# Kernel optimization log

Hardware: AMD Instinct MI355X
Metric: run time of the kernel (lower is better)

Reference implementation:

```python
import jax, jax.numpy as jnp
import numpy as np

NEG_SLOPE = 0.2

def leaky(x):
    return jnp.where(x >= 0, x, NEG_SLOPE * x)

def setup_inputs() -> dict:
    key = jax.random.key(0)
    ks = jax.random.split(key, 9)
    B, D, H = 2048, 128, 512
    s = lambda fan: 1.0 / np.sqrt(fan)
    return {
        "x":   jax.random.normal(ks[0], (B, D), jnp.float32),
        "We1": jax.random.normal(ks[1], (H, D), jnp.float32) * s(D),
        "be1": jax.random.normal(ks[2], (H,), jnp.float32) * s(D),
        "We2": jax.random.normal(ks[3], (D, H), jnp.float32) * s(H),
        "be2": jax.random.normal(ks[4], (D,), jnp.float32) * s(H),
        "W1s": jax.random.normal(ks[5], (D, H), jnp.float32),      # dec_j.linear1 weight (H,1) stacked -> (D,H)
        "b1s": jax.random.normal(ks[6], (D, H), jnp.float32) * 0.1,
        "W2s": jax.random.normal(ks[7], (D, D, H), jnp.float32) * s(H),  # dec_j.linear2 weight (D,H) stacked
        "b2s": jax.random.normal(ks[8], (D, D), jnp.float32) * s(H),
    }

def reference(x, We1, be1, We2, be2, W1s, b1s, W2s, b2s):
    # Encoder: D -> H -> D, tanh
    enc_h = leaky(x @ We1.T + be1)                     # (B,H)
    encoded = jnp.tanh(enc_h @ We2.T + be2)            # (B,D)
    # Per-feature decoders, vectorized over j: dec_j(encoded[:, j])
    z = encoded.T                                      # (D,B) latent scalar per decoder j
    hid = leaky(z[:, :, None] * W1s[:, None, :] + b1s[:, None, :])   # (D,B,H)
    terms = jnp.einsum('jbh,jdh->jbd', hid, W2s) + b2s[:, None, :]   # (D,B,D)
    # outputs[i] = sum_{j<=i} terms[j] -> inclusive prefix sum over j
    outputs = jnp.tanh(jnp.cumsum(terms, axis=0))      # (D,B,D)
    return outputs
```

## Files before the change

### kernel.cpp

```cpp
#include <hip/hip_runtime.h>

#define B_SZ 2048
#define D_SZ 128
#define H_SZ 512
#define JC 8
#define NCH 16
#define CPG 3
#define NGRP 5

typedef _Float16 half8 __attribute__((ext_vector_type(8)));
typedef float floatx4 __attribute__((ext_vector_type(4)));
typedef unsigned int uint4v __attribute__((ext_vector_type(4)));

static __device__ __forceinline__ float tanh_fast(float x) {
  float e = __expf(2.0f * x);
  return 1.0f - 2.0f * __builtin_amdgcn_rcpf(e + 1.0f);
}

static __device__ __forceinline__ void split_pair(float a, float b,
                                                  unsigned int& hi,
                                                  unsigned int& lo) {
  auto h = __builtin_amdgcn_cvt_pkrtz(a, b);
  float ra = a - (float)h[0];
  float rb = b - (float)h[1];
  auto l = __builtin_amdgcn_cvt_pkrtz(ra, rb);
  hi = __builtin_bit_cast(unsigned int, h);
  lo = __builtin_bit_cast(unsigned int, l);
}

__global__ __launch_bounds__(256) void prep_kernel(
    const float* __restrict__ W2s, _Float16* __restrict__ W2h,
    _Float16* __restrict__ W2l, const float* __restrict__ x,
    const float* __restrict__ We1, const float* __restrict__ be1,
    const float* __restrict__ We2, const float* __restrict__ be2,
    float* __restrict__ z) {
  const int t = threadIdx.x;
  if (blockIdx.x >= 256) {
    const int idx = (blockIdx.x - 256) * 256 + t;
    const int dl = idx & 63, kg = (idx >> 6) & 63, dtj = idx >> 12;
    const int d = (dtj & 1) * 64 + dl, j = dtj >> 1;
    const float* src = W2s + ((size_t)j * D_SZ + d) * H_SZ + kg * 8;
    float4 a = *(const float4*)src;
    float4 b = *(const float4*)(src + 4);
    unsigned int h0, l0, h1, l1, h2, l2, h3, l3;
    split_pair(a.x, a.y, h0, l0); split_pair(a.z, a.w, h1, l1);
    split_pair(b.x, b.y, h2, l2); split_pair(b.z, b.w, h3, l3);
    ((uint4*)W2h)[idx] = make_uint4(h0, h1, h2, h3);
    ((uint4*)W2l)[idx] = make_uint4(l0, l1, l2, l3);
    return;
  }
  __shared__ float xs[8][132];
  __shared__ float hs[8][516];
  const int b0 = blockIdx.x * 8;
  {
    int r = t >> 5, c4 = t & 31;
    float4 v = ((const float4*)(x + (size_t)(b0 + r) * D_SZ))[c4];
    xs[r][c4 * 4 + 0] = v.x; xs[r][c4 * 4 + 1] = v.y;
    xs[r][c4 * 4 + 2] = v.z; xs[r][c4 * 4 + 3] = v.w;
  }
  __syncthreads();
  for (int hb = 0; hb < 2; ++hb) {
    const int h = t + hb * 256;
    float acc[8];
    float bias = be1[h];
#pragma unroll
    for (int r = 0; r < 8; ++r) acc[r] = bias;
    const float4* wp = (const float4*)(We1 + (size_t)h * D_SZ);
    for (int k4 = 0; k4 < 32; ++k4) {
      float4 wv = wp[k4];
#pragma unroll
      for (int r = 0; r < 8; ++r) {
        acc[r] = fmaf(wv.x, xs[r][k4 * 4 + 0], acc[r]);
        acc[r] = fmaf(wv.y, xs[r][k4 * 4 + 1], acc[r]);
        acc[r] = fmaf(wv.z, xs[r][k4 * 4 + 2], acc[r]);
        acc[r] = fmaf(wv.w, xs[r][k4 * 4 + 3], acc[r]);
      }
    }
#pragma unroll
    for (int r = 0; r < 8; ++r) {
      float u = acc[r];
      hs[r][h] = fmaxf(u, 0.2f * u);
    }
  }
  __syncthreads();
  {
    const int d = t & 127, rg = t >> 7;
    float acc[4];
    float bias = be2[d];
#pragma unroll
    for (int r = 0; r < 4; ++r) acc[r] = bias;
    const float4* wp = (const float4*)(We2 + (size_t)d * H_SZ);
    for (int k4 = 0; k4 < 128; ++k4) {
      float4 wv = wp[k4];
#pragma unroll
      for (int r = 0; r < 4; ++r) {
        int row = rg * 4 + r;
        acc[r] = fmaf(wv.x, hs[row][k4 * 4 + 0], acc[r]);
        acc[r] = fmaf(wv.y, hs[row][k4 * 4 + 1], acc[r]);
        acc[r] = fmaf(wv.z, hs[row][k4 * 4 + 2], acc[r]);
        acc[r] = fmaf(wv.w, hs[row][k4 * 4 + 3], acc[r]);
      }
    }
#pragma unroll
    for (int r = 0; r < 4; ++r) {
      z[(size_t)d * B_SZ + b0 + rg * 4 + r] = tanh_fast(acc[r]);
    }
  }
}

__global__ __launch_bounds__(256, 2) void dec_kernel(
    const float* __restrict__ W1s, const float* __restrict__ b1s,
    const _Float16* __restrict__ W2h, const _Float16* __restrict__ W2l,
    const float* __restrict__ b2s, const float* __restrict__ z,
    float* __restrict__ out, float* __restrict__ T) {
  __shared__ float w1L[JC][512];
  __shared__ float b1L[JC][512];
  __shared__ float zL[JC][64];
  __shared__ float b2L[JC][128];
  __shared__ uint4v aHs[2][4][64];
  __shared__ uint4v aLs[2][4][64];

  const int t = threadIdx.x, bx = blockIdx.x;
  const int jc = bx & 15, bt = bx >> 4;
  const int b0 = bt * 64, j0 = jc * JC;

#pragma unroll
  for (int i = 0; i < 4; ++i) {
    int g = t + 256 * i;
    int jr = g >> 7, col = (g & 127) * 4;
    *(float4*)&w1L[jr][col] = *(const float4*)(W1s + (size_t)(j0 + jr) * H_SZ + col);
    *(float4*)&b1L[jr][col] = *(const float4*)(b1s + (size_t)(j0 + jr) * H_SZ + col);
  }
  if (t < 128) {
    int jr = t >> 4, col = (t & 15) * 4;
    *(float4*)&zL[jr][col] = *(const float4*)(z + (size_t)(j0 + jr) * B_SZ + b0 + col);
  }
  {
    int jr = t >> 5, col = (t & 31) * 4;
    *(float4*)&b2L[jr][col] = *(const float4*)(b2s + (size_t)(j0 + jr) * D_SZ + col);
  }
  __syncthreads();

  const int lane = t & 63;
  const int quad = lane >> 4, l16 = lane & 15;
  const int w = t >> 6;
  const int h = w & 1;
  const int pw = w ^ 1;

  floatx4 acc[2][4][3];
#pragma unroll
  for (int a = 0; a < 2; ++a)
#pragma unroll
    for (int b = 0; b < 4; ++b)
#pragma unroll
      for (int p = 0; p < 3; ++p) acc[a][b][p] = (floatx4){0.f, 0.f, 0.f, 0.f};
  float bc[4] = {0.f, 0.f, 0.f, 0.f};

  for (int jj = 0; jj < JC; ++jj) {
    const int j = j0 + jj;
    const unsigned int bb0 =
        (unsigned)(j * 2 + h) * 32768u + (unsigned)(quad * 512 + l16 * 8);
    const float zv = zL[jj][w * 16 + l16];

#pragma unroll 2
    for (int ks = 0; ks < 16; ++ks) {
      const int par = ks & 1;
      const unsigned int off = bb0 + (unsigned)(ks * 2048);
      half8 fh0 = *(const half8*)(W2h + off);
      half8 fh1 = *(const half8*)(W2h + off + 128);
      half8 fh2 = *(const half8*)(W2h + off + 256);
      half8 fh3 = *(const half8*)(W2h + off + 384);
      half8 fl0 = *(const half8*)(W2l + off);
      half8 fl1 = *(const half8*)(W2l + off + 128);
      half8 fl2 = *(const half8*)(W2l + off + 256);
      half8 fl3 = *(const half8*)(W2l + off + 384);

      const int ko = ks * 32 + quad * 8;
      float4 wa = *(const float4*)&w1L[jj][ko];
      float4 wc = *(const float4*)&w1L[jj][ko + 4];
      float4 ba = *(const float4*)&b1L[jj][ko];
      float4 bb = *(const float4*)&b1L[jj][ko + 4];

      float h0 = fmaf(zv, wa.x, ba.x), h1 = fmaf(zv, wa.y, ba.y);
      float h2 = fmaf(zv, wa.z, ba.z), h3 = fmaf(zv, wa.w, ba.w);
      float h4 = fmaf(zv, wc.x, bb.x), h5 = fmaf(zv, wc.y, bb.y);
      float h6 = fmaf(zv, wc.z, bb.z), h7 = fmaf(zv, wc.w, bb.w);
      h0 = fmaxf(h0, 0.2f * h0); h1 = fmaxf(h1, 0.2f * h1);
      h2 = fmaxf(h2, 0.2f * h2); h3 = fmaxf(h3, 0.2f * h3);
      h4 = fmaxf(h4, 0.2f * h4); h5 = fmaxf(h5, 0.2f * h5);
      h6 = fmaxf(h6, 0.2f * h6); h7 = fmaxf(h7, 0.2f * h7);
      unsigned int a0, a1, a2, a3, x0, x1, x2, x3;
      split_pair(h0, h1, a0, x0); split_pair(h2, h3, a1, x1);
      split_pair(h4, h5, a2, x2); split_pair(h6, h7, a3, x3);
      half8 fah = __builtin_bit_cast(half8, (uint4v){a0, a1, a2, a3});
      half8 fal = __builtin_bit_cast(half8, (uint4v){x0, x1, x2, x3});

      aHs[par][w][lane] = (uint4v){a0, a1, a2, a3};
      aLs[par][w][lane] = (uint4v){x0, x1, x2, x3};
      __syncthreads();
      half8 pah = __builtin_bit_cast(half8, aHs[par][pw][lane]);
      half8 pal = __builtin_bit_cast(half8, aLs[par][pw][lane]);

      acc[0][0][0] = __builtin_amdgcn_mfma_f32_16x16x32_f16(fah, fh0, acc[0][0][0], 0, 0, 0);
      acc[0][0][1] = __builtin_amdgcn_mfma_f32_16x16x32_f16(fah, fl0, acc[0][0][1], 0, 0, 0);
      acc[0][0][2] = __builtin_amdgcn_mfma_f32_16x16x32_f16(fal, fh0, acc[0][0][2], 0, 0, 0);
      acc[0][1][0] = __builtin_amdgcn_mfma_f32_16x16x32_f16(fah, fh1, acc[0][1][0], 0, 0, 0);
      acc[0][1][1] = __builtin_amdgcn_mfma_f32_16x16x32_f16(fah, fl1, acc[0][1][1], 0, 0, 0);
      acc[0][1][2] = __builtin_amdgcn_mfma_f32_16x16x32_f16(fal, fh1, acc[0][1][2], 0, 0, 0);
      acc[0][2][0] = __builtin_amdgcn_mfma_f32_16x16x32_f16(fah, fh2, acc[0][2][0], 0, 0, 0);
      acc[0][2][1] = __builtin_amdgcn_mfma_f32_16x16x32_f16(fah, fl2, acc[0][2][1], 0, 0, 0);
      acc[0][2][2] = __builtin_amdgcn_mfma_f32_16x16x32_f16(fal, fh2, acc[0][2][2], 0, 0, 0);
      acc[0][3][0] = __builtin_amdgcn_mfma_f32_16x16x32_f16(fah, fh3, acc[0][3][0], 0, 0, 0);
      acc[0][3][1] = __builtin_amdgcn_mfma_f32_16x16x32_f16(fah, fl3, acc[0][3][1], 0, 0, 0);
      acc[0][3][2] = __builtin_amdgcn_mfma_f32_16x16x32_f16(fal, fh3, acc[0][3][2], 0, 0, 0);
      acc[1][0][0] = __builtin_amdgcn_mfma_f32_16x16x32_f16(pah, fh0, acc[1][0][0], 0, 0, 0);
      acc[1][0][1] = __builtin_amdgcn_mfma_f32_16x16x32_f16(pah, fl0, acc[1][0][1], 0, 0, 0);
      acc[1][0][2] = __builtin_amdgcn_mfma_f32_16x16x32_f16(pal, fh0, acc[1][0][2], 0, 0, 0);
      acc[1][1][0] = __builtin_amdgcn_mfma_f32_16x16x32_f16(pah, fh1, acc[1][1][0], 0, 0, 0);
      acc[1][1][1] = __builtin_amdgcn_mfma_f32_16x16x32_f16(pah, fl1, acc[1][1][1], 0, 0, 0);
      acc[1][1][2] = __builtin_amdgcn_mfma_f32_16x16x32_f16(pal, fh1, acc[1][1][2], 0, 0, 0);
      acc[1][2][0] = __builtin_amdgcn_mfma_f32_16x16x32_f16(pah, fh2, acc[1][2][0], 0, 0, 0);
      acc[1][2][1] = __builtin_amdgcn_mfma_f32_16x16x32_f16(pah, fl2, acc[1][2][1], 0, 0, 0);
      acc[1][2][2] = __builtin_amdgcn_mfma_f32_16x16x32_f16(pal, fh2, acc[1][2][2], 0, 0, 0);
      acc[1][3][0] = __builtin_amdgcn_mfma_f32_16x16x32_f16(pah, fh3, acc[1][3][0], 0, 0, 0);
      acc[1][3][1] = __builtin_amdgcn_mfma_f32_16x16x32_f16(pah, fl3, acc[1][3][1], 0, 0, 0);
      acc[1][3][2] = __builtin_amdgcn_mfma_f32_16x16x32_f16(pal, fh3, acc[1][3][2], 0, 0, 0);
    }

#pragma unroll
    for (int df = 0; df < 4; ++df) bc[df] += b2L[jj][h * 64 + df * 16 + l16];

    const int dcol = h * 64 + l16;
    float* obase = out + (size_t)j * (B_SZ * D_SZ) + dcol;
#pragma unroll
    for (int bf = 0; bf < 2; ++bf) {
      const int rb = bf ? pw : w;
      const int brow = b0 + rb * 16 + quad * 4;
      float* orow = obase + (size_t)brow * D_SZ;
#pragma unroll
      for (int r = 0; r < 4; ++r) {
#pragma unroll
        for (int df = 0; df < 4; ++df) {
          float s = (acc[bf][df][0][r] + acc[bf][df][1][r]) +
                    (acc[bf][df][2][r] + bc[df]);
          if (jc == 0) s = tanh_fast(s);
          orow[(size_t)r * D_SZ + df * 16] = s;
        }
      }
    }
  }

  if (jc < NCH - 1) {
    const int dcol = h * 64 + l16;
    float* tbase = T + (size_t)jc * (B_SZ * D_SZ) + dcol;
#pragma unroll
    for (int bf = 0; bf < 2; ++bf) {
      const int rb = bf ? pw : w;
      const int brow = b0 + rb * 16 + quad * 4;
      float* trow = tbase + (size_t)brow * D_SZ;
#pragma unroll
      for (int r = 0; r < 4; ++r) {
#pragma unroll
        for (int df = 0; df < 4; ++df) {
          trow[(size_t)r * D_SZ + df * 16] =
              (acc[bf][df][0][r] + acc[bf][df][1][r]) +
              (acc[bf][df][2][r] + bc[df]);
        }
      }
    }
  }
}

__global__ __launch_bounds__(256) void fixup_kernel(
    const float* __restrict__ T, float* __restrict__ out) {
  const int idx = blockIdx.x * 256 + threadIdx.x;
  const int d4 = idx & 31;
  const int b = (idx >> 5) & (B_SZ - 1);
  const int q = idx >> 16;
  const size_t stride = B_SZ * (D_SZ / 4);
  const size_t tix = (size_t)b * (D_SZ / 4) + d4;
  const float4* T4 = (const float4*)T;
  float4* O4 = (float4*)out;

  const int c0 = 1 + q * CPG;
  float4 carry = make_float4(0.f, 0.f, 0.f, 0.f);
  for (int c = 0; c < c0; ++c) {
    float4 tv = T4[(size_t)c * stride + tix];
    carry.x += tv.x; carry.y += tv.y; carry.z += tv.z; carry.w += tv.w;
  }
#pragma unroll
  for (int cc = 0; cc < CPG; ++cc) {
    const int c = c0 + cc;
    if (cc > 0) {
      float4 tv = T4[(size_t)(c - 1) * stride + tix];
      carry.x += tv.x; carry.y += tv.y; carry.z += tv.z; carry.w += tv.w;
    }
#pragma unroll
    for (int jj = 0; jj < JC; ++jj) {
      const int j = c * JC + jj;
      const size_t oix = ((size_t)j * B_SZ + b) * (D_SZ / 4) + d4;
      float4 s = O4[oix];
      s.x = tanh_fast(s.x + carry.x);
      s.y = tanh_fast(s.y + carry.y);
      s.z = tanh_fast(s.z + carry.z);
      s.w = tanh_fast(s.w + carry.w);
      O4[oix] = s;
    }
  }
}

extern "C" void kernel_launch(void* const* d_in, const int* in_sizes, int n_in,
                              void* d_out, int out_size, void* d_ws,
                              size_t ws_size, hipStream_t stream) {
  (void)in_sizes; (void)n_in; (void)out_size; (void)ws_size;
  const float* x   = (const float*)d_in[0];
  const float* We1 = (const float*)d_in[1];
  const float* be1 = (const float*)d_in[2];
  const float* We2 = (const float*)d_in[3];
  const float* be2 = (const float*)d_in[4];
  const float* W1s = (const float*)d_in[5];
  const float* b1s = (const float*)d_in[6];
  const float* W2s = (const float*)d_in[7];
  const float* b2s = (const float*)d_in[8];
  float* out = (float*)d_out;

  float* zws = (float*)d_ws;
  _Float16* W2h = (_Float16*)((char*)d_ws + (1u << 20));
  _Float16* W2l = (_Float16*)((char*)d_ws + (1u << 20) + (1u << 24));
  float* T = (float*)((char*)d_ws + (1u << 20) + (2u << 24));

  prep_kernel<<<4352, 256, 0, stream>>>(W2s, W2h, W2l, x, We1, be1, We2, be2, zws);
  dec_kernel<<<512, 256, 0, stream>>>(W1s, b1s, W2h, W2l, b2s, zws, out, T);
  fixup_kernel<<<NGRP * 256, 256, 0, stream>>>(T, out);
}
```

Baseline: 340.8 us.

## Software-pipeline W2 fragment loads across flattened j/k loop and merge accumulators

Flattens the per-decoder and k-step loops into one 128-step loop and prefetches the next step's W2 hi/lo fragments and activation split one iteration ahead, so global loads and LDS exchange overlap the MFMAs of the current step. The two low-order correction accumulators are merged into one, cutting accumulator registers from 24 to 16 floatx4 sets, though the prefetch buffers add register pressure. The single barrier per step now covers the double-buffered LDS activation exchange for the next step.

```diff
diff --git a/kernel.cpp b/kernel.cpp
--- a/kernel.cpp
+++ b/kernel.cpp
@@ -146,41 +146,82 @@
   const int w = t >> 6;
   const int h = w & 1;
   const int pw = w ^ 1;
-
-  floatx4 acc[2][4][3];
+  const int rowL = w * 16 + l16;
+  const unsigned voff = (unsigned)(quad * 512 + l16 * 8);
+
+  floatx4 acc[2][4][2];
 #pragma unroll
   for (int a = 0; a < 2; ++a)
 #pragma unroll
     for (int b = 0; b < 4; ++b)
 #pragma unroll
-      for (int p = 0; p < 3; ++p) acc[a][b][p] = (floatx4){0.f, 0.f, 0.f, 0.f};
+      for (int p = 0; p < 2; ++p) acc[a][b][p] = (floatx4){0.f, 0.f, 0.f, 0.f};
   float bc[4] = {0.f, 0.f, 0.f, 0.f};
 
-  for (int jj = 0; jj < JC; ++jj) {
+  half8 curh, curl, cb[8];
+  {
+    const float zv = zL[0][rowL];
+    const int ko = quad * 8;
+    float4 wa = *(const float4*)&w1L[0][ko];
+    float4 wc = *(const float4*)&w1L[0][ko + 4];
+    float4 ba = *(const float4*)&b1L[0][ko];
+    float4 bb = *(const float4*)&b1L[0][ko + 4];
+    float h0 = fmaf(zv, wa.x, ba.x), h1 = fmaf(zv, wa.y, ba.y);
+    float h2 = fmaf(zv, wa.z, ba.z), h3 = fmaf(zv, wa.w, ba.w);
+    float h4 = fmaf(zv, wc.x, bb.x), h5 = fmaf(zv, wc.y, bb.y);
+    float h6 = fmaf(zv, wc.z, bb.z), h7 = fmaf(zv, wc.w, bb.w);
+    h0 = fmaxf(h0, 0.2f * h0); h1 = fmaxf(h1, 0.2f * h1);
+    h2 = fmaxf(h2, 0.2f * h2); h3 = fmaxf(h3, 0.2f * h3);
+    h4 = fmaxf(h4, 0.2f * h4); h5 = fmaxf(h5, 0.2f * h5);
+    h6 = fmaxf(h6, 0.2f * h6); h7 = fmaxf(h7, 0.2f * h7);
+    unsigned int a0, a1, a2, a3, x0, x1, x2, x3;
+    split_pair(h0, h1, a0, x0); split_pair(h2, h3, a1, x1);
+    split_pair(h4, h5, a2, x2); split_pair(h6, h7, a3, x3);
+    aHs[0][w][lane] = (uint4v){a0, a1, a2, a3};
+    aLs[0][w][lane] = (uint4v){x0, x1, x2, x3};
+    curh = __builtin_bit_cast(half8, (uint4v){a0, a1, a2, a3});
+    curl = __builtin_bit_cast(half8, (uint4v){x0, x1, x2, x3});
+    const unsigned off = (unsigned)(j0 * 2 + h) * 32768u + voff;
+    cb[0] = *(const half8*)(W2h + off);
+    cb[1] = *(const half8*)(W2h + off + 128);
+    cb[2] = *(const half8*)(W2h + off + 256);
+    cb[3] = *(const half8*)(W2h + off + 384);
+    cb[4] = *(const half8*)(W2l + off);
+    cb[5] = *(const half8*)(W2l + off + 128);
+    cb[6] = *(const half8*)(W2l + off + 256);
+    cb[7] = *(const half8*)(W2l + off + 384);
+  }
+  __syncthreads();
+
+#pragma unroll 2
+  for (int s = 0; s < 128; ++s) {
+    const int par = s & 1;
+    const int jj = s >> 4;
     const int j = j0 + jj;
-    const unsigned int bb0 =
-        (unsigned)(j * 2 + h) * 32768u + (unsigned)(quad * 512 + l16 * 8);
-    const float zv = zL[jj][w * 16 + l16];
-
-#pragma unroll 2
-    for (int ks = 0; ks < 16; ++ks) {
-      const int par = ks & 1;
-      const unsigned int off = bb0 + (unsigned)(ks * 2048);
-      half8 fh0 = *(const half8*)(W2h + off);
-      half8 fh1 = *(const half8*)(W2h + off + 128);
-      half8 fh2 = *(const half8*)(W2h + off + 256);
-      half8 fh3 = *(const half8*)(W2h + off + 384);
-      half8 fl0 = *(const half8*)(W2l + off);
-      half8 fl1 = *(const half8*)(W2l + off + 128);
-      half8 fl2 = *(const half8*)(W2l + off + 256);
-      half8 fl3 = *(const half8*)(W2l + off + 384);
-
-      const int ko = ks * 32 + quad * 8;
-      float4 wa = *(const float4*)&w1L[jj][ko];
-      float4 wc = *(const float4*)&w1L[jj][ko + 4];
-      float4 ba = *(const float4*)&b1L[jj][ko];
-      float4 bb = *(const float4*)&b1L[jj][ko + 4];
-
+
+    uint4v pH = aHs[par][pw][lane];
+    uint4v pL = aLs[par][pw][lane];
+
+    half8 nb[8], nh, nl;
+    if (s < 127) {
+      const int sn = s + 1;
+      const int jn = sn >> 4, kn = sn & 15;
+      const unsigned off = (unsigned)((j0 + jn) * 2 + h) * 32768u +
+                           (unsigned)(kn * 2048) + voff;
+      nb[0] = *(const half8*)(W2h + off);
+      nb[1] = *(const half8*)(W2h + off + 128);
+      nb[2] = *(const half8*)(W2h + off + 256);
+      nb[3] = *(const half8*)(W2h + off + 384);
+      nb[4] = *(const half8*)(W2l + off);
+      nb[5] = *(const half8*)(W2l + off + 128);
+      nb[6] = *(const half8*)(W2l + off + 256);
+      nb[7] = *(const half8*)(W2l + off + 384);
+      const float zv = zL[jn][rowL];
+      const int ko = kn * 32 + quad * 8;
+      float4 wa = *(const float4*)&w1L[jn][ko];
+      float4 wc = *(const float4*)&w1L[jn][ko + 4];
+      float4 ba = *(const float4*)&b1L[jn][ko];
+      float4 bb = *(const float4*)&b1L[jn][ko + 4];
       float h0 = fmaf(zv, wa.x, ba.x), h1 = fmaf(zv, wa.y, ba.y);
       float h2 = fmaf(zv, wa.z, ba.z), h3 = fmaf(zv, wa.w, ba.w);
       float h4 = fmaf(zv, wc.x, bb.x), h5 = fmaf(zv, wc.y, bb.y);
@@ -192,59 +233,49 @@
       unsigned int a0, a1, a2, a3, x0, x1, x2, x3;
       split_pair(h0, h1, a0, x0); split_pair(h2, h3, a1, x1);
       split_pair(h4, h5, a2, x2); split_pair(h6, h7, a3, x3);
-      half8 fah = __builtin_bit_cast(half8, (uint4v){a0, a1, a2, a3});
-      half8 fal = __builtin_bit_cast(half8, (uint4v){x0, x1, x2, x3});
-
-      aHs[par][w][lane] = (uint4v){a0, a1, a2, a3};
-      aLs[par][w][lane] = (uint4v){x0, x1, x2, x3};
-      __syncthreads();
-      half8 pah = __builtin_bit_cast(half8, aHs[par][pw][lane]);
-      half8 pal = __builtin_bit_cast(half8, aLs[par][pw][lane]);
-
-      acc[0][0][0] = __builtin_amdgcn_mfma_f32_16x16x32_f16(fah, fh0, acc[0][0][0], 0, 0, 0);
-      acc[0][0][1] = __builtin_amdgcn_mfma_f32_16x16x32_f16(fah, fl0, acc[0][0][1], 0, 0, 0);
-      acc[0][0][2] = __builtin_amdgcn_mfma_f32_16x16x32_f16(fal, fh0, acc[0][0][2], 0, 0, 0);
-      acc[0][1][0] = __builtin_amdgcn_mfma_f32_16x16x32_f16(fah, fh1, acc[0][1][0], 0, 0, 0);
-      acc[0][1][1] = __builtin_amdgcn_mfma_f32_16x16x32_f16(fah, fl1, acc[0][1][1], 0, 0, 0);
-      acc[0][1][2] = __builtin_amdgcn_mfma_f32_16x16x32_f16(fal, fh1, acc[0][1][2], 0, 0, 0);
-      acc[0][2][0] = __builtin_amdgcn_mfma_f32_16x16x32_f16(fah, fh2, acc[0][2][0], 0, 0, 0);
-      acc[0][2][1] = __builtin_amdgcn_mfma_f32_16x16x32_f16(fah, fl2, acc[0][2][1], 0, 0, 0);
-      acc[0][2][2] = __builtin_amdgcn_mfma_f32_16x16x32_f16(fal, fh2, acc[0][2][2], 0, 0, 0);
-      acc[0][3][0] = __builtin_amdgcn_mfma_f32_16x16x32_f16(fah, fh3, acc[0][3][0], 0, 0, 0);
-      acc[0][3][1] = __builtin_amdgcn_mfma_f32_16x16x32_f16(fah, fl3, acc[0][3][1], 0, 0, 0);
-      acc[0][3][2] = __builtin_amdgcn_mfma_f32_16x16x32_f16(fal, fh3, acc[0][3][2], 0, 0, 0);
-      acc[1][0][0] = __builtin_amdgcn_mfma_f32_16x16x32_f16(pah, fh0, acc[1][0][0], 0, 0, 0);
-      acc[1][0][1] = __builtin_amdgcn_mfma_f32_16x16x32_f16(pah, fl0, acc[1][0][1], 0, 0, 0);
-      acc[1][0][2] = __builtin_amdgcn_mfma_f32_16x16x32_f16(pal, fh0, acc[1][0][2], 0, 0, 0);
-      acc[1][1][0] = __builtin_amdgcn_mfma_f32_16x16x32_f16(pah, fh1, acc[1][1][0], 0, 0, 0);
-      acc[1][1][1] = __builtin_amdgcn_mfma_f32_16x16x32_f16(pah, fl1, acc[1][1][1], 0, 0, 0);
-      acc[1][1][2] = __builtin_amdgcn_mfma_f32_16x16x32_f16(pal, fh1, acc[1][1][2], 0, 0, 0);
-      acc[1][2][0] = __builtin_amdgcn_mfma_f32_16x16x32_f16(pah, fh2, acc[1][2][0], 0, 0, 0);
-      acc[1][2][1] = __builtin_amdgcn_mfma_f32_16x16x32_f16(pah, fl2, acc[1][2][1], 0, 0, 0);
-      acc[1][2][2] = __builtin_amdgcn_mfma_f32_16x16x32_f16(pal, fh2, acc[1][2][2], 0, 0, 0);
-      acc[1][3][0] = __builtin_amdgcn_mfma_f32_16x16x32_f16(pah, fh3, acc[1][3][0], 0, 0, 0);
-      acc[1][3][1] = __builtin_amdgcn_mfma_f32_16x16x32_f16(pah, fl3, acc[1][3][1], 0, 0, 0);
-      acc[1][3][2] = __builtin_amdgcn_mfma_f32_16x16x32_f16(pal, fh3, acc[1][3][2], 0, 0, 0);
-    }
-
-#pragma unroll
-    for (int df = 0; df < 4; ++df) bc[df] += b2L[jj][h * 64 + df * 16 + l16];
-
-    const int dcol = h * 64 + l16;
-    float* obase = out + (size_t)j * (B_SZ * D_SZ) + dcol;
-#pragma unroll
-    for (int bf = 0; bf < 2; ++bf) {
-      const int rb = bf ? pw : w;
-      const int brow = b0 + rb * 16 + quad * 4;
-      float* orow = obase + (size_t)brow * D_SZ;
-#pragma unroll
-      for (int r = 0; r < 4; ++r) {
-#pragma unroll
-        for (int df = 0; df < 4; ++df) {
-          float s = (acc[bf][df][0][r] + acc[bf][df][1][r]) +
-                    (acc[bf][df][2][r] + bc[df]);
-          if (jc == 0) s = tanh_fast(s);
-          orow[(size_t)r * D_SZ + df * 16] = s;
+      aHs[sn & 1][w][lane] = (uint4v){a0, a1, a2, a3};
+      aLs[sn & 1][w][lane] = (uint4v){x0, x1, x2, x3};
+      nh = __builtin_bit_cast(half8, (uint4v){a0, a1, a2, a3});
+      nl = __builtin_bit_cast(half8, (uint4v){x0, x1, x2, x3});
+    }
+    __syncthreads();
+    half8 pah = __builtin_bit_cast(half8, pH);
+    half8 pal = __builtin_bit_cast(half8, pL);
+
+#pragma unroll
+    for (int df = 0; df < 4; ++df) {
+      acc[0][df][0] = __builtin_amdgcn_mfma_f32_16x16x32_f16(curh, cb[df], acc[0][df][0], 0, 0, 0);
+      acc[0][df][1] = __builtin_amdgcn_mfma_f32_16x16x32_f16(curh, cb[df + 4], acc[0][df][1], 0, 0, 0);
+      acc[0][df][1] = __builtin_amdgcn_mfma_f32_16x16x32_f16(curl, cb[df], acc[0][df][1], 0, 0, 0);
+      acc[1][df][0] = __builtin_amdgcn_mfma_f32_16x16x32_f16(pah, cb[df], acc[1][df][0], 0, 0, 0);
+      acc[1][df][1] = __builtin_amdgcn_mfma_f32_16x16x32_f16(pah, cb[df + 4], acc[1][df][1], 0, 0, 0);
+      acc[1][df][1] = __builtin_amdgcn_mfma_f32_16x16x32_f16(pal, cb[df], acc[1][df][1], 0, 0, 0);
+    }
+
+    if (s < 127) {
+      curh = nh; curl = nl;
+#pragma unroll
+      for (int i = 0; i < 8; ++i) cb[i] = nb[i];
+    }
+
+    if ((s & 15) == 15) {
+#pragma unroll
+      for (int df = 0; df < 4; ++df) bc[df] += b2L[jj][h * 64 + df * 16 + l16];
+      const int dcol = h * 64 + l16;
+      float* obase = out + (size_t)j * (B_SZ * D_SZ) + dcol;
+#pragma unroll
+      for (int bf = 0; bf < 2; ++bf) {
+        const int rb = bf ? pw : w;
+        const int brow = b0 + rb * 16 + quad * 4;
+        float* orow = obase + (size_t)brow * D_SZ;
+#pragma unroll
+        for (int r = 0; r < 4; ++r) {
+#pragma unroll
+          for (int df = 0; df < 4; ++df) {
+            float sv = (acc[bf][df][0][r] + acc[bf][df][1][r]) + bc[df];
+            if (jc == 0) sv = tanh_fast(sv);
+            orow[(size_t)r * D_SZ + df * 16] = sv;
+          }
         }
       }
     }
@@ -263,8 +294,7 @@
 #pragma unroll
         for (int df = 0; df < 4; ++df) {
           trow[(size_t)r * D_SZ + df * 16] =
-              (acc[bf][df][0][r] + acc[bf][df][1][r]) +
-              (acc[bf][df][2][r] + bc[df]);
+              (acc[bf][df][0][r] + acc[bf][df][1][r]) + bc[df];
         }
       }
     }
```

Measured after the change: 351.6 us. +3.2%, slower.
